# Kernel optimization log

Hardware: AMD Instinct MI355X
Metric: run time of the kernel (lower is better)

The kernel has to match this reference:

```python
import jax, jax.numpy as jnp
import numpy as np

EMBED_DIM = 1024
NUM_HEADS = 16
HEAD_DIM = EMBED_DIM // NUM_HEADS


def setup_inputs() -> dict:
    key = jax.random.key(0)
    k_x, k_wqkv, k_bqkv, k_wp, k_bp = jax.random.split(key, 5)
    B, S = 4, 2048
    scale = 1.0 / np.sqrt(EMBED_DIM)
    return {
        "x": jax.random.normal(k_x, (B, S, EMBED_DIM), dtype=jnp.float32),
        "w_qkv": jax.random.uniform(k_wqkv, (EMBED_DIM, 3 * EMBED_DIM), jnp.float32, -scale, scale),
        "b_qkv": jax.random.uniform(k_bqkv, (3 * EMBED_DIM,), jnp.float32, -scale, scale),
        "w_proj": jax.random.uniform(k_wp, (EMBED_DIM, EMBED_DIM), jnp.float32, -scale, scale),
        "b_proj": jax.random.uniform(k_bp, (EMBED_DIM,), jnp.float32, -scale, scale),
    }


def reference(x, w_qkv, b_qkv, w_proj, b_proj):
    B, S, E = x.shape
    H, D = NUM_HEADS, HEAD_DIM
    # fused QKV projection: [B,S,3E] -> [3,B,H,S,D]
    qkv = (x @ w_qkv + b_qkv).reshape(B, S, 3, H, D).transpose(2, 0, 3, 1, 4)
    q, k, v = qkv[0], qkv[1], qkv[2]
    scores = jnp.einsum("bhqd,bhkd->bhqk", q, k) / np.sqrt(D).astype(jnp.float32)
    attn = jax.nn.softmax(scores, axis=-1)  # dropout is identity in eval
    out = jnp.einsum("bhqk,bhkd->bhqd", attn, v)
    out = out.transpose(0, 2, 1, 3).reshape(B, S, E)
    return out @ w_proj + b_proj
```

## Files before the change

### kernel.cpp

```cpp
#include <hip/hip_runtime.h>
#include <hip/hip_bf16.h>

#define PB 4
#define PS 2048
#define PH 16
#define PD 64
#define PE 1024

typedef short v8s __attribute__((ext_vector_type(8)));
typedef float v4f __attribute__((ext_vector_type(4)));

#define QSCALE 0.18033688f

__device__ __forceinline__ ushort f2b(float f) {
  union { __hip_bfloat16 b; ushort u; } cv;
  cv.b = __float2bfloat16(f);
  return cv.u;
}

#if __has_builtin(__builtin_amdgcn_exp2f)
__device__ __forceinline__ float fexp2(float x) { return __builtin_amdgcn_exp2f(x); }
#else
__device__ __forceinline__ float fexp2(float x) { return exp2f(x); }
#endif

__device__ __forceinline__ void cp16(const __hip_bfloat16* g, __hip_bfloat16* l) {
  __builtin_amdgcn_global_load_lds(
      (const __attribute__((address_space(1))) void*)g,
      (__attribute__((address_space(3))) void*)l, 16, 0, 0);
}

__device__ __forceinline__ int xcd_swz(int orig, int nwg) {
  return (orig & 7) * (nwg >> 3) + (orig >> 3);
}

__global__ __launch_bounds__(256) void conv_f2b(const float* __restrict__ S,
                                                __hip_bfloat16* __restrict__ D) {
  int i = blockIdx.x * 256 + threadIdx.x;
  float4 f = reinterpret_cast<const float4*>(S)[i];
  union { ushort u[4]; uint2 v; } pk;
  pk.u[0] = f2b(f.x); pk.u[1] = f2b(f.y); pk.u[2] = f2b(f.z); pk.u[3] = f2b(f.w);
  reinterpret_cast<uint2*>(D)[i] = pk.v;
}

__global__ __launch_bounds__(256) void transp_f2b(const float* __restrict__ S,
                                                  __hip_bfloat16* __restrict__ D,
                                                  int R, int C) {
  __shared__ float tile[32][33];
  const int t = threadIdx.x;
  const int tx = t & 31, ty = t >> 5;
  const int r0 = blockIdx.y * 32, c0 = blockIdx.x * 32;
#pragma unroll
  for (int i = 0; i < 4; ++i)
    tile[ty + 8 * i][tx] = S[(size_t)(r0 + ty + 8 * i) * C + c0 + tx];
  __syncthreads();
#pragma unroll
  for (int i = 0; i < 4; ++i)
    D[(size_t)(c0 + ty + 8 * i) * R + r0 + tx] = __float2bfloat16(tile[tx][ty + 8 * i]);
}

template <int MODE>
__global__ __launch_bounds__(256) void gemm_bt(
    const __hip_bfloat16* __restrict__ A, const __hip_bfloat16* __restrict__ BT,
    const float* __restrict__ bias, void* __restrict__ outv) {
  __shared__ __hip_bfloat16 As[128 * 64];
  __shared__ __hip_bfloat16 Bs[128 * 64];
  const int t = threadIdx.x;
  const int lane = t & 63, w = t >> 6;
  const int ln = lane & 15, qd = lane >> 4;
  const int wm = w >> 1, wn = w & 1;
  const int gx = gridDim.x;
  const int swz = xcd_swz(blockIdx.y * gx + blockIdx.x, gx * gridDim.y);
  const int m0 = (swz / gx) * 128, n0 = (swz % gx) * 128;
  v4f acc[4][4] = {};

  for (int k0 = 0; k0 < PE; k0 += 64) {
    __syncthreads();
#pragma unroll
    for (int i = 0; i < 4; ++i) {
      int idx = t + 256 * i;
      int r = idx >> 3, cs = idx & 7;
      int cg = cs ^ (r & 7);
      cp16(A + (size_t)(m0 + r) * PE + k0 + cg * 8, As + idx * 8);
      cp16(BT + (size_t)(n0 + r) * PE + k0 + cg * 8, Bs + idx * 8);
    }
    __syncthreads();
#pragma unroll
    for (int kk = 0; kk < 2; ++kk) {
      v8s af[4], bf[4];
#pragma unroll
      for (int mb = 0; mb < 4; ++mb) {
        int ra = wm * 64 + mb * 16 + ln;
        int ca = (kk * 4 + qd) ^ (ra & 7);
        af[mb] = *reinterpret_cast<const v8s*>(As + ra * 64 + ca * 8);
      }
#pragma unroll
      for (int nb = 0; nb < 4; ++nb) {
        int rb = wn * 64 + nb * 16 + ln;
        int cb = (kk * 4 + qd) ^ (rb & 7);
        bf[nb] = *reinterpret_cast<const v8s*>(Bs + rb * 64 + cb * 8);
      }
#pragma unroll
      for (int mb = 0; mb < 4; ++mb)
#pragma unroll
        for (int nb = 0; nb < 4; ++nb)
          acc[mb][nb] = __builtin_amdgcn_mfma_f32_16x16x32_bf16(af[mb], bf[nb],
                                                                acc[mb][nb], 0, 0, 0);
    }
  }

  const int mwb = m0 + wm * 64 + qd * 4;
  const int nwb = n0 + wn * 64 + ln;
  if (MODE == 0) {
    __hip_bfloat16* QKV = (__hip_bfloat16*)outv;
#pragma unroll
    for (int nb = 0; nb < 4; ++nb) {
      int n = nwb + nb * 16;
      float bv = bias[n];
      int which = n >> 10, h = (n >> 6) & 15, d = n & 63;
#pragma unroll
      for (int mb = 0; mb < 4; ++mb) {
        int r0 = mwb + mb * 16;
        int b = r0 >> 11, s0 = r0 & (PS - 1);
        v4f a = acc[mb][nb];
        if (which == 2) {
          union { ushort u[4]; uint2 v; } pk;
#pragma unroll
          for (int i = 0; i < 4; ++i) pk.u[i] = f2b(a[i] + bv);
          size_t idx = (((size_t)(2 * PB + b) * PH + h) * PD + d) * PS + s0;
          *reinterpret_cast<uint2*>(&QKV[idx]) = pk.v;
        } else {
          float sc = (which == 0) ? QSCALE : 1.0f;
          size_t base = (((size_t)(which * PB + b) * PH + h) * PS + s0) * PD + d;
#pragma unroll
          for (int i = 0; i < 4; ++i)
            QKV[base + (size_t)i * PD] = __float2bfloat16((a[i] + bv) * sc);
        }
      }
    }
  } else {
    float* Co = (float*)outv;
#pragma unroll
    for (int nb = 0; nb < 4; ++nb) {
      int n = nwb + nb * 16;
      float bv = bias[n];
#pragma unroll
      for (int mb = 0; mb < 4; ++mb) {
        int r0 = mwb + mb * 16;
        v4f a = acc[mb][nb];
#pragma unroll
        for (int i = 0; i < 4; ++i)
          Co[(size_t)(r0 + i) * PE + n] = a[i] + bv;
      }
    }
  }
}

__global__ __launch_bounds__(256) void attn_mfma8(
    const __hip_bfloat16* __restrict__ QKV, __hip_bfloat16* __restrict__ O) {
  __shared__ __hip_bfloat16 Ks[64 * 64];
  __shared__ __hip_bfloat16 Vts[64 * 64];
  const int t = threadIdx.x;
  const int lane = t & 63, w = t >> 6;
  const int ln = lane & 15, qd = lane >> 4;
  const int swz = xcd_swz(blockIdx.y * 16 + blockIdx.x, 16 * 64);
  const int bx = swz & 15, by = swz >> 4;
  const int b = by >> 4, h = by & 15;
  const int q0 = bx * 128;
  const __hip_bfloat16* Qb = QKV + (size_t)(b * PH + h) * PS * PD;
  const __hip_bfloat16* Kb = QKV + (size_t)((PB + b) * PH + h) * PS * PD;
  const __hip_bfloat16* Vb = QKV + (size_t)((2 * PB + b) * PH + h) * PD * PS;

  v8s qf[2][2];
#pragma unroll
  for (int u = 0; u < 2; ++u) {
    size_t qr = (size_t)(q0 + 32 * w + 16 * u + ln) * PD;
    qf[u][0] = *reinterpret_cast<const v8s*>(Qb + qr + qd * 8);
    qf[u][1] = *reinterpret_cast<const v8s*>(Qb + qr + 32 + qd * 8);
  }
  v4f oacc[2][4] = {};
  float lrow[2] = {0.f, 0.f};

  const int r7 = ln & 7;
  const int c0 = qd ^ r7;
  const int q1 = qd & 1, qh = qd >> 1;
  int soff[2][2];
#pragma unroll
  for (int s = 0; s < 2; ++s) {
    int L0 = 4 * s + qh;
    soff[s][0] = (((L0 ^ r7) << 1) | q1);
    soff[s][1] = ((((L0 + 2) ^ r7) << 1) | q1);
  }
  int rvoff[4];
#pragma unroll
  for (int db = 0; db < 4; ++db) rvoff[db] = (db * 16 + ln) * 16;

  const int sr0 = t >> 3, sc0 = t & 7;
  const int sr1 = (t + 256) >> 3, sc1 = t & 7;
  const int dk0 = sr0 * 8 + (sc0 ^ (sr0 & 7));
  const int dk1 = sr1 * 8 + (sc1 ^ (sr1 & 7));

  v8s kreg[2], vreg[2];
  auto LOADR = [&](int kt) {
    kreg[0] = *reinterpret_cast<const v8s*>(Kb + (size_t)(kt + sr0) * PD + sc0 * 8);
    vreg[0] = *reinterpret_cast<const v8s*>(Vb + (size_t)sr0 * PS + kt + sc0 * 8);
    kreg[1] = *reinterpret_cast<const v8s*>(Kb + (size_t)(kt + sr1) * PD + sc1 * 8);
    vreg[1] = *reinterpret_cast<const v8s*>(Vb + (size_t)sr1 * PS + kt + sc1 * 8);
  };
  auto DSWR = [&]() {
    *reinterpret_cast<v8s*>(Ks + dk0 * 8) = kreg[0];
    *reinterpret_cast<v8s*>(Vts + dk0 * 8) = vreg[0];
    *reinterpret_cast<v8s*>(Ks + dk1 * 8) = kreg[1];
    *reinterpret_cast<v8s*>(Vts + dk1 * 8) = vreg[1];
  };

  auto COMPUTE = [&]() {
    const __hip_bfloat16* Kbuf = Ks;
    const uint2* Vbuf = reinterpret_cast<const uint2*>(Vts);
    uint2 pw[2][4];
#pragma unroll
    for (int u = 0; u < 2; ++u) {
      float psum = 0.f;
#pragma unroll
      for (int nb = 0; nb < 4; ++nb) {
        const __hip_bfloat16* kr = Kbuf + (nb * 16 + ln) * 64;
        v8s k0 = *reinterpret_cast<const v8s*>(kr + c0 * 8);
        v8s k1 = *reinterpret_cast<const v8s*>(kr + (c0 ^ 4) * 8);
        v4f z = {};
        z = __builtin_amdgcn_mfma_f32_16x16x32_bf16(k0, qf[u][0], z, 0, 0, 0);
        v4f sv = __builtin_amdgcn_mfma_f32_16x16x32_bf16(k1, qf[u][1], z, 0, 0, 0);
        union { ushort pu[4]; uint2 pv; } pk;
#pragma unroll
        for (int i = 0; i < 4; ++i) {
          float p = fexp2(sv[i]);
          psum += p;
          pk.pu[i] = f2b(p);
        }
        pw[u][nb] = pk.pv;
      }
      psum += __shfl_xor(psum, 16);
      psum += __shfl_xor(psum, 32);
      lrow[u] += psum;
    }
#pragma unroll
    for (int s = 0; s < 2; ++s) {
      union { v8s v; uint2 u2[2]; } a0, a1;
      a0.u2[0] = pw[0][2 * s]; a0.u2[1] = pw[0][2 * s + 1];
      a1.u2[0] = pw[1][2 * s]; a1.u2[1] = pw[1][2 * s + 1];
      __builtin_amdgcn_s_setprio(1);
#pragma unroll
      for (int db = 0; db < 4; ++db) {
        union { v8s v; uint2 u2[2]; } vf;
        vf.u2[0] = Vbuf[rvoff[db] + soff[s][0]];
        vf.u2[1] = Vbuf[rvoff[db] + soff[s][1]];
        oacc[0][db] = __builtin_amdgcn_mfma_f32_16x16x32_bf16(a0.v, vf.v,
                                                              oacc[0][db], 0, 0, 0);
        oacc[1][db] = __builtin_amdgcn_mfma_f32_16x16x32_bf16(a1.v, vf.v,
                                                              oacc[1][db], 0, 0, 0);
      }
      __builtin_amdgcn_s_setprio(0);
    }
  };

  const int NT = PS / 64;
  LOADR(0);
  DSWR();
  __syncthreads();
#pragma unroll 1
  for (int it = 0; it < NT; ++it) {
    if (it + 1 < NT) LOADR((it + 1) * 64);
    COMPUTE();
    __syncthreads();
    if (it + 1 < NT) DSWR();
    __syncthreads();
  }

#pragma unroll
  for (int u = 0; u < 2; ++u) {
#pragma unroll
    for (int i = 0; i < 4; ++i) {
      float inv = 1.f / __shfl(lrow[u], qd * 4 + i);
      int sg = q0 + 32 * w + 16 * u + qd * 4 + i;
      size_t base = (((size_t)b * PS + sg) * PH + h) * PD;
#pragma unroll
      for (int db = 0; db < 4; ++db)
        O[base + db * 16 + ln] = __float2bfloat16(oacc[u][db][i] * inv);
    }
  }
}

__device__ __forceinline__ uint2 load4bf(const float* p) {
  const float4 f = *reinterpret_cast<const float4*>(p);
  union { ushort u[4]; uint2 v; } pk;
  pk.u[0] = f2b(f.x); pk.u[1] = f2b(f.y); pk.u[2] = f2b(f.z); pk.u[3] = f2b(f.w);
  return pk.v;
}
__device__ __forceinline__ uint2 load4bf(const __hip_bfloat16* p) {
  return *reinterpret_cast<const uint2*>(p);
}

template <typename AT, int MODE>
__global__ __launch_bounds__(256) void gemm128(
    const AT* __restrict__ A, const float* __restrict__ Bm,
    const float* __restrict__ bias, void* __restrict__ outv, int ldb) {
  __shared__ __hip_bfloat16 As[128][40];
  __shared__ __hip_bfloat16 Bs[128][40];
  const int t = threadIdx.x;
  const int lane = t & 63, w = t >> 6;
  const int ln = lane & 15, qd = lane >> 4;
  const int wm = w >> 1, wn = w & 1;
  const int m0 = blockIdx.y * 128, n0 = blockIdx.x * 128;
  v4f acc[4][4] = {};
  for (int k0 = 0; k0 < PE; k0 += 32) {
    __syncthreads();
#pragma unroll
    for (int i = 0; i < 4; ++i) {
      int p = t + 256 * i;
      int m = p >> 3, kc = p & 7;
      *reinterpret_cast<uint2*>(&As[m][kc * 4]) =
          load4bf(A + (size_t)(m0 + m) * PE + k0 + kc * 4);
    }
#pragma unroll
    for (int i = 0; i < 4; ++i) {
      int p = t + 256 * i;
      int n = p & 127, kc = p >> 7;
      union { ushort u[4]; uint2 v; } pk;
#pragma unroll
      for (int r = 0; r < 4; ++r)
        pk.u[r] = f2b(Bm[(size_t)(k0 + kc * 4 + r) * ldb + n0 + n]);
      *reinterpret_cast<uint2*>(&Bs[n][kc * 4]) = pk.v;
    }
    __syncthreads();
    v8s af[4], bf[4];
#pragma unroll
    for (int mb = 0; mb < 4; ++mb)
      af[mb] = *reinterpret_cast<const v8s*>(&As[wm * 64 + mb * 16 + ln][qd * 8]);
#pragma unroll
    for (int nb = 0; nb < 4; ++nb)
      bf[nb] = *reinterpret_cast<const v8s*>(&Bs[wn * 64 + nb * 16 + ln][qd * 8]);
#pragma unroll
    for (int mb = 0; mb < 4; ++mb)
#pragma unroll
      for (int nb = 0; nb < 4; ++nb)
        acc[mb][nb] = __builtin_amdgcn_mfma_f32_16x16x32_bf16(af[mb], bf[nb],
                                                              acc[mb][nb], 0, 0, 0);
  }
  const int mwb = m0 + wm * 64 + qd * 4;
  const int nwb = n0 + wn * 64 + ln;
  if (MODE == 0) {
    __hip_bfloat16* QKV = (__hip_bfloat16*)outv;
#pragma unroll
    for (int nb = 0; nb < 4; ++nb) {
      int n = nwb + nb * 16;
      float bv = bias[n];
      int which = n >> 10, h = (n >> 6) & 15, d = n & 63;
#pragma unroll
      for (int mb = 0; mb < 4; ++mb) {
        int r0 = mwb + mb * 16;
        int b = r0 >> 11, s0 = r0 & (PS - 1);
        v4f a = acc[mb][nb];
        if (which == 2) {
          union { ushort u[4]; uint2 v; } pk;
#pragma unroll
          for (int i = 0; i < 4; ++i) pk.u[i] = f2b(a[i] + bv);
          size_t idx = (((size_t)(2 * PB + b) * PH + h) * PD + d) * PS + s0;
          *reinterpret_cast<uint2*>(&QKV[idx]) = pk.v;
        } else {
          float sc = (which == 0) ? QSCALE : 1.0f;
          size_t base = (((size_t)(which * PB + b) * PH + h) * PS + s0) * PD + d;
#pragma unroll
          for (int i = 0; i < 4; ++i)
            QKV[base + (size_t)i * PD] = __float2bfloat16((a[i] + bv) * sc);
        }
      }
    }
  } else {
    float* Co = (float*)outv;
#pragma unroll
    for (int nb = 0; nb < 4; ++nb) {
      int n = nwb + nb * 16;
      float bv = bias[n];
#pragma unroll
      for (int mb = 0; mb < 4; ++mb) {
        int r0 = mwb + mb * 16;
        v4f a = acc[mb][nb];
#pragma unroll
        for (int i = 0; i < 4; ++i)
          Co[(size_t)(r0 + i) * PE + n] = a[i] + bv;
      }
    }
  }
}

extern "C" void kernel_launch(void* const* d_in, const int* in_sizes, int n_in,
                              void* d_out, int out_size, void* d_ws,
                              size_t ws_size, hipStream_t stream) {
  const float* x = (const float*)d_in[0];
  const float* w_qkv = (const float*)d_in[1];
  const float* b_qkv = (const float*)d_in[2];
  const float* w_proj = (const float*)d_in[3];
  const float* b_proj = (const float*)d_in[4];
  float* out = (float*)d_out;

  const size_t xE = (size_t)PB * PS * PE;
  const size_t wqE = (size_t)PE * 3 * PE;
  const size_t wpE = (size_t)PE * PE;
  const size_t qkvE = (size_t)3 * PB * PH * PS * PD;
  const size_t needMain = (xE + wqE + wpE + qkvE) * 2;

  dim3 blk(256);
  dim3 gq(24, 64), ga(16, 64), gp(8, 64);

  if (ws_size >= needMain) {
    __hip_bfloat16* xb = (__hip_bfloat16*)d_ws;
    __hip_bfloat16* wqkvT = xb + xE;
    __hip_bfloat16* wprojT = wqkvT + wqE;
    __hip_bfloat16* qkv = wprojT + wpE;
    __hip_bfloat16* o = xb;

    conv_f2b<<<dim3(xE / 1024), blk, 0, stream>>>(x, xb);
    transp_f2b<<<dim3(96, 32), blk, 0, stream>>>(w_qkv, wqkvT, PE, 3 * PE);
    transp_f2b<<<dim3(32, 32), blk, 0, stream>>>(w_proj, wprojT, PE, PE);
    gemm_bt<0><<<gq, blk, 0, stream>>>(xb, wqkvT, b_qkv, qkv);
    attn_mfma8<<<ga, blk, 0, stream>>>(qkv, o);
    gemm_bt<1><<<gp, blk, 0, stream>>>(o, wprojT, b_proj, out);
  } else {
    __hip_bfloat16* qkv = (__hip_bfloat16*)d_ws;
    if (ws_size >= (qkvE + xE) * 2) {
      __hip_bfloat16* o = qkv + qkvE;
      gemm128<float, 0><<<gq, blk, 0, stream>>>(x, w_qkv, b_qkv, qkv, 3 * PE);
      attn_mfma8<<<ga, blk, 0, stream>>>(qkv, o);
      gemm128<__hip_bfloat16, 1><<<gp, blk, 0, stream>>>(o, w_proj, b_proj, out, PE);
    } else {
      __hip_bfloat16* o = (__hip_bfloat16*)d_out;
      float* tmp = (float*)d_ws;
      gemm128<float, 0><<<gq, blk, 0, stream>>>(x, w_qkv, b_qkv, qkv, 3 * PE);
      attn_mfma8<<<ga, blk, 0, stream>>>(qkv, o);
      gemm128<__hip_bfloat16, 1><<<gp, blk, 0, stream>>>(o, w_proj, b_proj, tmp, PE);
      hipMemcpyAsync(d_out, tmp, xE * sizeof(float), hipMemcpyDeviceToDevice, stream);
    }
  }
}
```

Before: 284.9 us.

## Use 256x256-tile double-buffered 8-wave GEMM for QKV projection

Replaces the 128x128 QKV projection GEMM with a new 512-thread kernel that computes 256x256 output tiles. It double-buffers swizzled LDS tiles loaded asynchronously with global_load_lds and interleaves prefetch of the next K slice with MFMA work. It also raises wave priority around the MFMA blocks. Larger tiles increase operand reuse and cut global traffic, at the cost of 128KB of LDS per block (one block per CU) and a grid of only 384 blocks, which may leave tail imbalance.

```diff
diff --git a/kernel.cpp b/kernel.cpp
--- a/kernel.cpp
+++ b/kernel.cpp
@@ -28,6 +28,12 @@
   __builtin_amdgcn_global_load_lds(
       (const __attribute__((address_space(1))) void*)g,
       (__attribute__((address_space(3))) void*)l, 16, 0, 0);
+}
+
+__device__ __forceinline__ void barrier_fence() {
+  asm volatile("" ::: "memory");
+  __builtin_amdgcn_s_barrier();
+  asm volatile("" ::: "memory");
 }
 
 __device__ __forceinline__ int xcd_swz(int orig, int nwg) {
@@ -57,6 +63,107 @@
 #pragma unroll
   for (int i = 0; i < 4; ++i)
     D[(size_t)(c0 + ty + 8 * i) * R + r0 + tx] = __float2bfloat16(tile[tx][ty + 8 * i]);
+}
+
+__global__ __launch_bounds__(512) void gemm256(
+    const __hip_bfloat16* __restrict__ A, const __hip_bfloat16* __restrict__ BT,
+    const float* __restrict__ bias, __hip_bfloat16* __restrict__ QKV) {
+  __shared__ __hip_bfloat16 As[2][256 * 64];
+  __shared__ __hip_bfloat16 Bs[2][256 * 64];
+  const int t = threadIdx.x;
+  const int lane = t & 63, w = t >> 6;
+  const int ln = lane & 15, qd = lane >> 4;
+  const int wr = w >> 2, wc = w & 3;
+  const int gx = gridDim.x;
+  const int swz = xcd_swz(blockIdx.y * gx + blockIdx.x, gx * gridDim.y);
+  const int m0 = (swz / gx) * 256, n0 = (swz % gx) * 256;
+  v4f acc[8][4] = {};
+
+  auto STAGE = [&](int buf, int k0, int p) {
+    int idx = t + p * 512;
+    int r = idx >> 3, cs = idx & 7;
+    int cg = cs ^ (r & 7);
+    cp16(A + (size_t)(m0 + r) * PE + k0 + cg * 8, As[buf] + idx * 8);
+    cp16(BT + (size_t)(n0 + r) * PE + k0 + cg * 8, Bs[buf] + idx * 8);
+  };
+
+#pragma unroll
+  for (int p = 0; p < 4; ++p) STAGE(0, 0, p);
+  asm volatile("s_waitcnt vmcnt(0)" ::: "memory");
+  barrier_fence();
+
+#pragma unroll 1
+  for (int tl = 0; tl < 16; ++tl) {
+    const int buf = tl & 1;
+    const __hip_bfloat16* Ab = As[buf];
+    const __hip_bfloat16* Bb = Bs[buf];
+    const int k1 = (tl + 1) * 64;
+#pragma unroll
+    for (int p = 0; p < 4; ++p) {
+      v8s af[2][2], bf[4][2];
+#pragma unroll
+      for (int m = 0; m < 2; ++m) {
+        int ra = wr * 128 + (p * 2 + m) * 16 + ln;
+#pragma unroll
+        for (int kk = 0; kk < 2; ++kk) {
+          int ca = (kk * 4 + qd) ^ (ra & 7);
+          af[m][kk] = *reinterpret_cast<const v8s*>(Ab + ra * 64 + ca * 8);
+        }
+      }
+#pragma unroll
+      for (int nb = 0; nb < 4; ++nb) {
+        int rb = wc * 64 + nb * 16 + ln;
+#pragma unroll
+        for (int kk = 0; kk < 2; ++kk) {
+          int cb = (kk * 4 + qd) ^ (rb & 7);
+          bf[nb][kk] = *reinterpret_cast<const v8s*>(Bb + rb * 64 + cb * 8);
+        }
+      }
+      if (tl < 15) STAGE(buf ^ 1, k1, p);
+      barrier_fence();
+      __builtin_amdgcn_s_setprio(1);
+#pragma unroll
+      for (int kk = 0; kk < 2; ++kk)
+#pragma unroll
+        for (int m = 0; m < 2; ++m)
+#pragma unroll
+          for (int nb = 0; nb < 4; ++nb)
+            acc[p * 2 + m][nb] = __builtin_amdgcn_mfma_f32_16x16x32_bf16(
+                af[m][kk], bf[nb][kk], acc[p * 2 + m][nb], 0, 0, 0);
+      __builtin_amdgcn_s_setprio(0);
+      barrier_fence();
+    }
+    asm volatile("s_waitcnt vmcnt(0)" ::: "memory");
+    barrier_fence();
+  }
+
+  const int mwb = m0 + wr * 128 + qd * 4;
+  const int nwb = n0 + wc * 64 + ln;
+#pragma unroll
+  for (int nb = 0; nb < 4; ++nb) {
+    int n = nwb + nb * 16;
+    float bv = bias[n];
+    int which = n >> 10, h = (n >> 6) & 15, d = n & 63;
+#pragma unroll
+    for (int mb = 0; mb < 8; ++mb) {
+      int r0 = mwb + mb * 16;
+      int b = r0 >> 11, s0 = r0 & (PS - 1);
+      v4f a = acc[mb][nb];
+      if (which == 2) {
+        union { ushort u[4]; uint2 v; } pk;
+#pragma unroll
+        for (int i = 0; i < 4; ++i) pk.u[i] = f2b(a[i] + bv);
+        size_t idx = (((size_t)(2 * PB + b) * PH + h) * PD + d) * PS + s0;
+        *reinterpret_cast<uint2*>(&QKV[idx]) = pk.v;
+      } else {
+        float sc = (which == 0) ? QSCALE : 1.0f;
+        size_t base = (((size_t)(which * PB + b) * PH + h) * PS + s0) * PD + d;
+#pragma unroll
+        for (int i = 0; i < 4; ++i)
+          QKV[base + (size_t)i * PD] = __float2bfloat16((a[i] + bv) * sc);
+      }
+    }
+  }
 }
 
 template <int MODE>
@@ -409,7 +516,8 @@
   const size_t needMain = (xE + wqE + wpE + qkvE) * 2;
 
   dim3 blk(256);
-  dim3 gq(24, 64), ga(16, 64), gp(8, 64);
+  dim3 gq256(12, 32), ga(16, 64), gp(8, 64);
+  dim3 gq(24, 64);
 
   if (ws_size >= needMain) {
     __hip_bfloat16* xb = (__hip_bfloat16*)d_ws;
@@ -421,7 +529,7 @@
     conv_f2b<<<dim3(xE / 1024), blk, 0, stream>>>(x, xb);
     transp_f2b<<<dim3(96, 32), blk, 0, stream>>>(w_qkv, wqkvT, PE, 3 * PE);
     transp_f2b<<<dim3(32, 32), blk, 0, stream>>>(w_proj, wprojT, PE, PE);
-    gemm_bt<0><<<gq, blk, 0, stream>>>(xb, wqkvT, b_qkv, qkv);
+    gemm256<<<gq256, dim3(512), 0, stream>>>(xb, wqkvT, b_qkv, qkv);
     attn_mfma8<<<ga, blk, 0, stream>>>(qkv, o);
     gemm_bt<1><<<gp, blk, 0, stream>>>(o, wprojT, b_proj, out);
   } else {
```

New measurement: 296.5 us. +4.1%, slower.
